# Kernel tuning notes

Measured on AMD Instinct MI355X. Metric: run time of the kernel, lower is better.

## Reference

```python
import jax, jax.numpy as jnp
import numpy as np

GAMMA = 5.0 / 3.0
N, H = 131072, 256


def mlp(c, W1, b1, W2, b2, W3, b3, W4, b4):
    h = jnp.tanh(c @ W1 + b1)
    h = jnp.tanh(h @ W2 + b2)
    h = jnp.tanh(h @ W3 + b3)
    return h @ W4 + b4  # [N, 6] -> (rho, vx, vy, Bx, By, P)


def setup_inputs() -> dict:
    key = jax.random.key(0)
    ks = jax.random.split(key, 6)
    s = 0.5
    return {
        "coords": jax.random.uniform(ks[0], (N, 3), jnp.float32),  # (x, y, t)
        "W1": jax.random.normal(ks[1], (3, H), jnp.float32) * s,
        "b1": jnp.zeros((H,), jnp.float32),
        "W2": jax.random.normal(ks[2], (H, H), jnp.float32) * (s / np.sqrt(H)),
        "b2": jnp.zeros((H,), jnp.float32),
        "W3": jax.random.normal(ks[3], (H, H), jnp.float32) * (s / np.sqrt(H)),
        "b3": jnp.zeros((H,), jnp.float32),
        "W4": jax.random.normal(ks[4], (H, 6), jnp.float32) * (s / np.sqrt(H)),
        "b4": jnp.zeros((6,), jnp.float32),
        "weights": jnp.ones((7,), jnp.float32),
    }


def reference(coords, W1, b1, W2, b2, W3, b3, W4, b4, weights):
    f = lambda c: mlp(c, W1, b1, W2, b2, W3, b3, W4, b4)
    preds = f(coords)
    # Batched Jacobian d preds / d coords via 3 forward-mode JVPs (basis dirs x,y,t)
    eye = jnp.eye(3, dtype=coords.dtype)
    jvp1 = lambda e: jax.jvp(f, (coords,), (jnp.broadcast_to(e, coords.shape),))[1]
    J = jnp.transpose(jax.vmap(jvp1)(eye), (1, 2, 0))  # [N, 6, 3]

    rho, vx, vy, Bx, By, P = (preds[:, k] for k in range(6))
    Jx, Jy, Jt = J[..., 0], J[..., 1], J[..., 2]  # each [N, 6]

    # time derivatives (chain rule for composite fields)
    dt_rho = Jt[:, 0]
    dt_Bx, dt_By = Jt[:, 3], Jt[:, 4]
    dt_rhovx = dt_rho * vx + rho * Jt[:, 1]
    dt_rhovy = dt_rho * vy + rho * Jt[:, 2]

    def dE(Jc):  # derivative of total energy E along coord c
        return (Jc[:, 5] / (GAMMA - 1.0)
                + 0.5 * Jc[:, 0] * (vx ** 2 + vy ** 2)
                + rho * (vx * Jc[:, 1] + vy * Jc[:, 2])
                + Bx * Jc[:, 3] + By * Jc[:, 4])

    dE_dx, dE_dy, dE_dt = dE(Jx), dE(Jy), dE(Jt)

    div_v = Jx[:, 1] + Jy[:, 2]
    div_B = Jx[:, 3] + Jy[:, 4]
    continuity = dt_rho + rho * div_v

    # grad of total pressure P + 0.5*(Bx^2 + By^2)
    dPm_dx = Jx[:, 5] + Bx * Jx[:, 3] + By * Jx[:, 4]
    dPm_dy = Jy[:, 5] + Bx * Jy[:, 3] + By * Jy[:, 4]
    momentum_x = dt_rhovx + dPm_dx - (Bx * Jx[:, 3] + By * Jy[:, 3])
    momentum_y = dt_rhovy + dPm_dy - (Bx * Jx[:, 4] + By * Jy[:, 4])

    # induction: G = vx*By - vy*Bx
    def dG(Jc):
        return Jc[:, 1] * By + vx * Jc[:, 4] - Jc[:, 2] * Bx - vy * Jc[:, 3]

    induction_x = dt_Bx + dG(Jy)
    induction_y = dt_By - dG(Jx)

    # energy: d/dt E + div( S*v - D*B ), S = E + P + Pm, D = B.v
    E = P / (GAMMA - 1.0) + 0.5 * rho * (vx ** 2 + vy ** 2) + 0.5 * (Bx ** 2 + By ** 2)
    S = E + P + 0.5 * (Bx ** 2 + By ** 2)
    dS_dx = dE_dx + Jx[:, 5] + Bx * Jx[:, 3] + By * Jx[:, 4]
    dS_dy = dE_dy + Jy[:, 5] + Bx * Jy[:, 3] + By * Jy[:, 4]
    D = Bx * vx + By * vy

    def dD(Jc):
        return Jc[:, 3] * vx + Bx * Jc[:, 1] + Jc[:, 4] * vy + By * Jc[:, 2]

    dFx_dx = dS_dx * vx + S * Jx[:, 1] - dD(Jx) * Bx - D * Jx[:, 3]
    dFy_dy = dS_dy * vy + S * Jy[:, 2] - dD(Jy) * By - D * Jy[:, 4]
    energy = dE_dt + dFx_dx + dFy_dy

    res = [continuity, momentum_x, momentum_y, induction_x, induction_y, energy, div_B]
    loss = sum(w * jnp.mean(r ** 2) for w, r in zip(weights, res))
    return loss
```

## Files before the change

kernel.cpp:

```cpp
#include <hip/hip_runtime.h>
#include <hip/hip_bf16.h>
#include <cstdint>


#define LDW 264
#define TPTS 16
#define GRIDB 256

typedef __attribute__((ext_vector_type(8))) short v8h;
typedef __attribute__((ext_vector_type(4))) float v4f;

__device__ __forceinline__ ushort f2b(float f) {
    uint32_t u = __float_as_uint(f);
    u = (u + 0x7fffu + ((u >> 16) & 1u)) >> 16;
    return (ushort)u;
}
__device__ __forceinline__ uint32_t pk2(float a, float b) {
    union { __hip_bfloat162 h2; uint32_t u; } cv;
    cv.h2 = __float22bfloat162_rn(make_float2(a, b));
    return cv.u;
}
__device__ __forceinline__ float fast_tanh(float x) {
    float e = __expf(2.0f * x);
    return 1.0f - 2.0f * __builtin_amdgcn_rcpf(e + 1.0f);
}

__global__ void prep_weights(const float* __restrict__ W2, const float* __restrict__ W3,
                             const float* __restrict__ W4,
                             ushort* __restrict__ Wt2, ushort* __restrict__ Wt3,
                             ushort* __restrict__ Wt4) {
    int idx = blockIdx.x * 256 + threadIdx.x;
    if (idx < 65536) {
        int k = idx >> 8, n = idx & 255;
        Wt2[n * 256 + k] = f2b(W2[k * 256 + n]);
        Wt3[n * 256 + k] = f2b(W3[k * 256 + n]);
    }
    if (idx < 4096) {
        int n = idx >> 8, k = idx & 255;
        Wt4[n * 256 + k] = (n < 6) ? f2b(W4[k * 6 + n]) : (ushort)0;
    }
}

__device__ __forceinline__ void dense_layer(const ushort* __restrict__ src,
                                            ushort* __restrict__ dst,
                                            const v8h (*wf)[8], const v4f* bs,
                                            int wv, int q, int l15) {
    v4f acc[2][4];
    #pragma unroll
    for (int a = 0; a < 2; a++)
        #pragma unroll
        for (int b = 0; b < 4; b++) {
            v4f z = {0.0f, 0.0f, 0.0f, 0.0f};
            acc[a][b] = z;
        }
    #pragma unroll
    for (int kk = 0; kk < 8; kk++) {
        v8h B[4];
        #pragma unroll
        for (int nt = 0; nt < 4; nt++)
            B[nt] = *(const v8h*)(&src[(nt * 16 + l15) * LDW + kk * 32 + q * 8]);
        #pragma unroll
        for (int mt = 0; mt < 2; mt++)
            #pragma unroll
            for (int nt = 0; nt < 4; nt++)
                acc[mt][nt] = __builtin_amdgcn_mfma_f32_16x16x32_bf16(wf[mt][kk], B[nt], acc[mt][nt], 0, 0, 0);
    }
    #pragma unroll
    for (int mt = 0; mt < 2; mt++) {
        const int colb = wv * 32 + mt * 16 + q * 4;
        v4f bb = bs[mt];
        float h0 = fast_tanh(acc[mt][0][0] + bb[0]);
        float h1 = fast_tanh(acc[mt][0][1] + bb[1]);
        float h2 = fast_tanh(acc[mt][0][2] + bb[2]);
        float h3 = fast_tanh(acc[mt][0][3] + bb[3]);
        float d0 = 1.0f - h0 * h0, d1 = 1.0f - h1 * h1;
        float d2 = 1.0f - h2 * h2, d3 = 1.0f - h3 * h3;
        uint2 w;
        w.x = pk2(h0, h1); w.y = pk2(h2, h3);
        *(uint2*)(&dst[l15 * LDW + colb]) = w;
        #pragma unroll
        for (int s = 1; s < 4; s++) {
            w.x = pk2(d0 * acc[mt][s][0], d1 * acc[mt][s][1]);
            w.y = pk2(d2 * acc[mt][s][2], d3 * acc[mt][s][3]);
            *(uint2*)(&dst[(s * 16 + l15) * LDW + colb]) = w;
        }
    }
}

__global__ __launch_bounds__(512, 2)
void mhd_fused(const float* __restrict__ coords,
               const float* __restrict__ W1, const float* __restrict__ b1,
               const float* __restrict__ b2, const float* __restrict__ b3,
               const float* __restrict__ b4,
               const float* __restrict__ wts,
               const ushort* __restrict__ Wt2, const ushort* __restrict__ Wt3,
               const ushort* __restrict__ Wt4,
               float* __restrict__ out, int npts, float inv_n) {
    __shared__ ushort Xs0[64 * LDW];
    __shared__ ushort Xs1[64 * LDW];
    __shared__ ushort W4s[16 * LDW];
    __shared__ float  cs[TPTS * 3];
    __shared__ float  Y4[4][TPTS][8];

    const int tid  = threadIdx.x;
    const int lane = tid & 63;
    const int wv   = tid >> 6;
    const int q    = lane >> 4;
    const int l15  = lane & 15;

    for (int idx = tid; idx < 16 * 256; idx += 512)
        W4s[(idx >> 8) * LDW + (idx & 255)] = Wt4[idx];

    v8h w2f[2][8], w3f[2][8];
    v4f bs2[2], bs3[2];
    #pragma unroll
    for (int mt = 0; mt < 2; mt++) {
        const int nrow = (wv * 32 + mt * 16 + l15) * 256 + q * 8;
        #pragma unroll
        for (int kk = 0; kk < 8; kk++) {
            w2f[mt][kk] = *(const v8h*)(&Wt2[nrow + kk * 32]);
            w3f[mt][kk] = *(const v8h*)(&Wt3[nrow + kk * 32]);
        }
        bs2[mt] = *(const v4f*)(&b2[wv * 32 + mt * 16 + q * 4]);
        bs3[mt] = *(const v4f*)(&b3[wv * 32 + mt * 16 + q * 4]);
    }

    const int jj = tid & 255, ph = tid >> 8;
    const float l1w0 = W1[jj], l1w1 = W1[256 + jj], l1w2 = W1[512 + jj], l1b = b1[jj];
    const float b40 = b4[0], b41 = b4[1], b42 = b4[2], b43 = b4[3], b44 = b4[4], b45 = b4[5];
    const float wt0 = wts[0], wt1 = wts[1], wt2_ = wts[2], wt3_ = wts[3],
                wt4_ = wts[4], wt5 = wts[5], wt6 = wts[6];

    const int ntiles = (npts + TPTS - 1) / TPTS;
    float vsum = 0.0f;

    for (int tile = blockIdx.x; tile < ntiles; tile += GRIDB) {
        const int base = tile * TPTS;

        if (tid < TPTS * 3) {
            int p = tid / 3, c = tid % 3;
            int gp = base + p; if (gp >= npts) gp = npts - 1;
            cs[tid] = coords[gp * 3 + c];
        }
        __syncthreads();

        #pragma unroll
        for (int pp = 0; pp < 8; pp++) {
            const int p = ph * 8 + pp;
            float x = cs[p * 3], y = cs[p * 3 + 1], t = cs[p * 3 + 2];
            float pre = fmaf(x, l1w0, fmaf(y, l1w1, fmaf(t, l1w2, l1b)));
            float h = fast_tanh(pre);
            float d = 1.0f - h * h;
            Xs0[p * LDW + jj]        = f2b(h);
            Xs0[(16 + p) * LDW + jj] = f2b(d * l1w0);
            Xs0[(32 + p) * LDW + jj] = f2b(d * l1w1);
            Xs0[(48 + p) * LDW + jj] = f2b(d * l1w2);
        }
        __syncthreads();

        dense_layer(Xs0, Xs1, w2f, bs2, wv, q, l15);
        __syncthreads();
        dense_layer(Xs1, Xs0, w3f, bs3, wv, q, l15);
        __syncthreads();

        if (wv < 4) {
            v4f a4 = {0.0f, 0.0f, 0.0f, 0.0f};
            #pragma unroll
            for (int kk = 0; kk < 8; kk++) {
                v8h A = *(const v8h*)(&W4s[l15 * LDW + kk * 32 + q * 8]);
                v8h B = *(const v8h*)(&Xs0[(wv * 16 + l15) * LDW + kk * 32 + q * 8]);
                a4 = __builtin_amdgcn_mfma_f32_16x16x32_bf16(A, B, a4, 0, 0, 0);
            }
            if (q < 2) {
                #pragma unroll
                for (int r = 0; r < 4; r++)
                    Y4[wv][l15][q * 4 + r] = a4[r];
            }
        }
        __syncthreads();

        if (tid < 16 && (base + tid) < npts) {
            const float* Yh = Y4[0][tid];
            const float* JX = Y4[1][tid];
            const float* JY = Y4[2][tid];
            const float* JT = Y4[3][tid];
            const float g1 = 1.5f;
            float rho = Yh[0] + b40, vx = Yh[1] + b41, vy = Yh[2] + b42;
            float Bx  = Yh[3] + b43, By = Yh[4] + b44, P  = Yh[5] + b45;
            float v2 = vx * vx + vy * vy;
            float dt_rho = JT[0];
            float dt_rhovx = dt_rho * vx + rho * JT[1];
            float dt_rhovy = dt_rho * vy + rho * JT[2];
            auto dE = [&](const float* J) {
                return J[5] * g1 + 0.5f * J[0] * v2 + rho * (vx * J[1] + vy * J[2]) + Bx * J[3] + By * J[4];
            };
            float dE_dx = dE(JX), dE_dy = dE(JY), dE_dt = dE(JT);
            float div_v = JX[1] + JY[2];
            float div_B = JX[3] + JY[4];
            float continuity = dt_rho + rho * div_v;
            float dPm_dx = JX[5] + Bx * JX[3] + By * JX[4];
            float dPm_dy = JY[5] + Bx * JY[3] + By * JY[4];
            float momentum_x = dt_rhovx + dPm_dx - (Bx * JX[3] + By * JY[3]);
            float momentum_y = dt_rhovy + dPm_dy - (Bx * JX[4] + By * JY[4]);
            auto dG = [&](const float* J) {
                return J[1] * By + vx * J[4] - J[2] * Bx - vy * J[3];
            };
            float induction_x = JT[3] + dG(JY);
            float induction_y = JT[4] - dG(JX);
            float E = P * g1 + 0.5f * rho * v2 + 0.5f * (Bx * Bx + By * By);
            float S = E + P + 0.5f * (Bx * Bx + By * By);
            float dS_dx = dE_dx + JX[5] + Bx * JX[3] + By * JX[4];
            float dS_dy = dE_dy + JY[5] + Bx * JY[3] + By * JY[4];
            float D = Bx * vx + By * vy;
            auto dD = [&](const float* J) {
                return J[3] * vx + Bx * J[1] + J[4] * vy + By * J[2];
            };
            float dFx_dx = dS_dx * vx + S * JX[1] - dD(JX) * Bx - D * JX[3];
            float dFy_dy = dS_dy * vy + S * JY[2] - dD(JY) * By - D * JY[4];
            float energy = dE_dt + dFx_dx + dFy_dy;
            vsum += wt0 * continuity * continuity
                  + wt1 * momentum_x * momentum_x
                  + wt2_ * momentum_y * momentum_y
                  + wt3_ * induction_x * induction_x
                  + wt4_ * induction_y * induction_y
                  + wt5 * energy * energy
                  + wt6 * div_B * div_B;
        }
    }

    if (tid < 64) {
        #pragma unroll
        for (int off = 8; off >= 1; off >>= 1)
            vsum += __shfl_down(vsum, off, 64);
        if (tid == 0) atomicAdd(out, vsum * inv_n);
    }
}

extern "C" void kernel_launch(void* const* d_in, const int* in_sizes, int n_in,
                              void* d_out, int out_size, void* d_ws, size_t ws_size,
                              hipStream_t stream) {
    const float* coords = (const float*)d_in[0];
    const float* W1 = (const float*)d_in[1];
    const float* b1 = (const float*)d_in[2];
    const float* W2 = (const float*)d_in[3];
    const float* b2 = (const float*)d_in[4];
    const float* W3 = (const float*)d_in[5];
    const float* b3 = (const float*)d_in[6];
    const float* W4 = (const float*)d_in[7];
    const float* b4 = (const float*)d_in[8];
    const float* wts = (const float*)d_in[9];
    const int npts = in_sizes[0] / 3;

    ushort* Wt2 = (ushort*)d_ws;
    ushort* Wt3 = Wt2 + 65536;
    ushort* Wt4 = Wt3 + 65536;

    hipMemsetAsync(d_out, 0, sizeof(float), stream);
    prep_weights<<<256, 256, 0, stream>>>(W2, W3, W4, Wt2, Wt3, Wt4);
    mhd_fused<<<GRIDB, 512, 0, stream>>>(coords, W1, b1, b2, b3, b4, wts,
                                         Wt2, Wt3, Wt4, (float*)d_out, npts, 1.0f / npts);
}
```

Before: 247.9 us.

## Pipeline layers 2 and 3 across warp groups with double-buffered activations

Splits the 8 waves into two groups: waves 0-3 compute layer 2 for tile i while waves 4-7 compute layer 3 for tile i-1, each group holding only its own layer's weights in registers (64 output columns per wave). Layer-2 output is double-buffered in LDS, and the next tile's coordinates are prefetched during the layer-4 stage. This cuts the number of barriers per tile and removes the serial layer2→layer3 dependency. In exchange it uses more LDS (4 activation buffers instead of 2), which may reduce occupancy, and adds a pipeline prologue and epilogue iteration.

New measurement: 259.5 us. 1.05x slower.

```diff
diff --git a/kernel.cpp b/kernel.cpp
--- a/kernel.cpp
+++ b/kernel.cpp
@@ -41,52 +41,6 @@
     }
 }
 
-__device__ __forceinline__ void dense_layer(const ushort* __restrict__ src,
-                                            ushort* __restrict__ dst,
-                                            const v8h (*wf)[8], const v4f* bs,
-                                            int wv, int q, int l15) {
-    v4f acc[2][4];
-    #pragma unroll
-    for (int a = 0; a < 2; a++)
-        #pragma unroll
-        for (int b = 0; b < 4; b++) {
-            v4f z = {0.0f, 0.0f, 0.0f, 0.0f};
-            acc[a][b] = z;
-        }
-    #pragma unroll
-    for (int kk = 0; kk < 8; kk++) {
-        v8h B[4];
-        #pragma unroll
-        for (int nt = 0; nt < 4; nt++)
-            B[nt] = *(const v8h*)(&src[(nt * 16 + l15) * LDW + kk * 32 + q * 8]);
-        #pragma unroll
-        for (int mt = 0; mt < 2; mt++)
-            #pragma unroll
-            for (int nt = 0; nt < 4; nt++)
-                acc[mt][nt] = __builtin_amdgcn_mfma_f32_16x16x32_bf16(wf[mt][kk], B[nt], acc[mt][nt], 0, 0, 0);
-    }
-    #pragma unroll
-    for (int mt = 0; mt < 2; mt++) {
-        const int colb = wv * 32 + mt * 16 + q * 4;
-        v4f bb = bs[mt];
-        float h0 = fast_tanh(acc[mt][0][0] + bb[0]);
-        float h1 = fast_tanh(acc[mt][0][1] + bb[1]);
-        float h2 = fast_tanh(acc[mt][0][2] + bb[2]);
-        float h3 = fast_tanh(acc[mt][0][3] + bb[3]);
-        float d0 = 1.0f - h0 * h0, d1 = 1.0f - h1 * h1;
-        float d2 = 1.0f - h2 * h2, d3 = 1.0f - h3 * h3;
-        uint2 w;
-        w.x = pk2(h0, h1); w.y = pk2(h2, h3);
-        *(uint2*)(&dst[l15 * LDW + colb]) = w;
-        #pragma unroll
-        for (int s = 1; s < 4; s++) {
-            w.x = pk2(d0 * acc[mt][s][0], d1 * acc[mt][s][1]);
-            w.y = pk2(d2 * acc[mt][s][2], d3 * acc[mt][s][3]);
-            *(uint2*)(&dst[(s * 16 + l15) * LDW + colb]) = w;
-        }
-    }
-}
-
 __global__ __launch_bounds__(512, 2)
 void mhd_fused(const float* __restrict__ coords,
                const float* __restrict__ W1, const float* __restrict__ b1,
@@ -96,8 +50,9 @@
                const ushort* __restrict__ Wt2, const ushort* __restrict__ Wt3,
                const ushort* __restrict__ Wt4,
                float* __restrict__ out, int npts, float inv_n) {
-    __shared__ ushort Xs0[64 * LDW];
-    __shared__ ushort Xs1[64 * LDW];
+    __shared__ ushort XsA[64 * LDW];
+    __shared__ ushort XsB[2][64 * LDW];
+    __shared__ ushort XsC[64 * LDW];
     __shared__ ushort W4s[16 * LDW];
     __shared__ float  cs[TPTS * 3];
     __shared__ float  Y4[4][TPTS][8];
@@ -107,124 +62,182 @@
     const int wv   = tid >> 6;
     const int q    = lane >> 4;
     const int l15  = lane & 15;
+    const int g3   = wv >> 2;
+    const int wvg  = wv & 3;
 
     for (int idx = tid; idx < 16 * 256; idx += 512)
         W4s[(idx >> 8) * LDW + (idx & 255)] = Wt4[idx];
 
-    v8h w2f[2][8], w3f[2][8];
-    v4f bs2[2], bs3[2];
+    const ushort* Wsrc = g3 ? Wt3 : Wt2;
+    const float*  bsrc = g3 ? b3  : b2;
+    v8h wf[4][8];
     #pragma unroll
-    for (int mt = 0; mt < 2; mt++) {
-        const int nrow = (wv * 32 + mt * 16 + l15) * 256 + q * 8;
+    for (int mt = 0; mt < 4; mt++) {
+        const int nrow = (wvg * 64 + mt * 16 + l15) * 256 + q * 8;
         #pragma unroll
-        for (int kk = 0; kk < 8; kk++) {
-            w2f[mt][kk] = *(const v8h*)(&Wt2[nrow + kk * 32]);
-            w3f[mt][kk] = *(const v8h*)(&Wt3[nrow + kk * 32]);
-        }
-        bs2[mt] = *(const v4f*)(&b2[wv * 32 + mt * 16 + q * 4]);
-        bs3[mt] = *(const v4f*)(&b3[wv * 32 + mt * 16 + q * 4]);
+        for (int kk = 0; kk < 8; kk++)
+            wf[mt][kk] = *(const v8h*)(&Wsrc[nrow + kk * 32]);
     }
 
     const int jj = tid & 255, ph = tid >> 8;
     const float l1w0 = W1[jj], l1w1 = W1[256 + jj], l1w2 = W1[512 + jj], l1b = b1[jj];
-    const float b40 = b4[0], b41 = b4[1], b42 = b4[2], b43 = b4[3], b44 = b4[4], b45 = b4[5];
-    const float wt0 = wts[0], wt1 = wts[1], wt2_ = wts[2], wt3_ = wts[3],
-                wt4_ = wts[4], wt5 = wts[5], wt6 = wts[6];
 
     const int ntiles = (npts + TPTS - 1) / TPTS;
+    const int nt_blk = (ntiles > (int)blockIdx.x)
+                         ? (ntiles - (int)blockIdx.x + GRIDB - 1) / GRIDB : 0;
+
     float vsum = 0.0f;
 
-    for (int tile = blockIdx.x; tile < ntiles; tile += GRIDB) {
-        const int base = tile * TPTS;
-
-        if (tid < TPTS * 3) {
-            int p = tid / 3, c = tid % 3;
-            int gp = base + p; if (gp >= npts) gp = npts - 1;
-            cs[tid] = coords[gp * 3 + c];
+    if (tid < TPTS * 3 && nt_blk > 0) {
+        int p = tid / 3, c = tid % 3;
+        int gp = (int)blockIdx.x * TPTS + p; if (gp >= npts) gp = npts - 1;
+        cs[tid] = coords[gp * 3 + c];
+    }
+    __syncthreads();
+
+    for (int i = 0; i <= nt_blk; ++i) {
+        const int base = ((int)blockIdx.x + i * GRIDB) * TPTS;
+
+        if (i < nt_blk) {
+            #pragma unroll
+            for (int pp = 0; pp < 8; pp++) {
+                const int p = ph * 8 + pp;
+                float x = cs[p * 3], y = cs[p * 3 + 1], t = cs[p * 3 + 2];
+                float pre = fmaf(x, l1w0, fmaf(y, l1w1, fmaf(t, l1w2, l1b)));
+                float h = fast_tanh(pre);
+                float d = 1.0f - h * h;
+                XsA[p * LDW + jj]        = f2b(h);
+                XsA[(16 + p) * LDW + jj] = f2b(d * l1w0);
+                XsA[(32 + p) * LDW + jj] = f2b(d * l1w1);
+                XsA[(48 + p) * LDW + jj] = f2b(d * l1w2);
+            }
         }
         __syncthreads();
 
-        #pragma unroll
-        for (int pp = 0; pp < 8; pp++) {
-            const int p = ph * 8 + pp;
-            float x = cs[p * 3], y = cs[p * 3 + 1], t = cs[p * 3 + 2];
-            float pre = fmaf(x, l1w0, fmaf(y, l1w1, fmaf(t, l1w2, l1b)));
-            float h = fast_tanh(pre);
-            float d = 1.0f - h * h;
-            Xs0[p * LDW + jj]        = f2b(h);
-            Xs0[(16 + p) * LDW + jj] = f2b(d * l1w0);
-            Xs0[(32 + p) * LDW + jj] = f2b(d * l1w1);
-            Xs0[(48 + p) * LDW + jj] = f2b(d * l1w2);
+        {
+            const ushort* src = g3 ? XsB[(i + 1) & 1] : XsA;
+            ushort*       dst = g3 ? XsC : XsB[i & 1];
+            const bool act = g3 ? (i >= 1) : (i < nt_blk);
+            if (act) {
+                v4f acc[4][4];
+                #pragma unroll
+                for (int a = 0; a < 4; a++)
+                    #pragma unroll
+                    for (int b = 0; b < 4; b++) {
+                        v4f z = {0.0f, 0.0f, 0.0f, 0.0f};
+                        acc[a][b] = z;
+                    }
+                #pragma unroll
+                for (int kk = 0; kk < 8; kk++) {
+                    v8h B[4];
+                    #pragma unroll
+                    for (int nt = 0; nt < 4; nt++)
+                        B[nt] = *(const v8h*)(&src[(nt * 16 + l15) * LDW + kk * 32 + q * 8]);
+                    #pragma unroll
+                    for (int mt = 0; mt < 4; mt++)
+                        #pragma unroll
+                        for (int nt = 0; nt < 4; nt++)
+                            acc[mt][nt] = __builtin_amdgcn_mfma_f32_16x16x32_bf16(
+                                              wf[mt][kk], B[nt], acc[mt][nt], 0, 0, 0);
+                }
+                #pragma unroll
+                for (int mt = 0; mt < 4; mt++) {
+                    const int nb = wvg * 64 + mt * 16 + q * 4;
+                    v4f bb = *(const v4f*)(&bsrc[nb]);
+                    float h0 = fast_tanh(acc[mt][0][0] + bb[0]);
+                    float h1 = fast_tanh(acc[mt][0][1] + bb[1]);
+                    float h2 = fast_tanh(acc[mt][0][2] + bb[2]);
+                    float h3 = fast_tanh(acc[mt][0][3] + bb[3]);
+                    float d0 = 1.0f - h0 * h0, d1 = 1.0f - h1 * h1;
+                    float d2 = 1.0f - h2 * h2, d3 = 1.0f - h3 * h3;
+                    uint2 w;
+                    w.x = pk2(h0, h1); w.y = pk2(h2, h3);
+                    *(uint2*)(&dst[l15 * LDW + nb]) = w;
+                    #pragma unroll
+                    for (int s = 1; s < 4; s++) {
+                        w.x = pk2(d0 * acc[mt][s][0], d1 * acc[mt][s][1]);
+                        w.y = pk2(d2 * acc[mt][s][2], d3 * acc[mt][s][3]);
+                        *(uint2*)(&dst[(s * 16 + l15) * LDW + nb]) = w;
+                    }
+                }
+            }
         }
         __syncthreads();
 
-        dense_layer(Xs0, Xs1, w2f, bs2, wv, q, l15);
-        __syncthreads();
-        dense_layer(Xs1, Xs0, w3f, bs3, wv, q, l15);
-        __syncthreads();
-
-        if (wv < 4) {
+        if (g3 && i >= 1) {
             v4f a4 = {0.0f, 0.0f, 0.0f, 0.0f};
             #pragma unroll
             for (int kk = 0; kk < 8; kk++) {
-                v8h A = *(const v8h*)(&W4s[l15 * LDW + kk * 32 + q * 8]);
-                v8h B = *(const v8h*)(&Xs0[(wv * 16 + l15) * LDW + kk * 32 + q * 8]);
-                a4 = __builtin_amdgcn_mfma_f32_16x16x32_bf16(A, B, a4, 0, 0, 0);
+                v8h A  = *(const v8h*)(&W4s[l15 * LDW + kk * 32 + q * 8]);
+                v8h Bf = *(const v8h*)(&XsC[(wvg * 16 + l15) * LDW + kk * 32 + q * 8]);
+                a4 = __builtin_amdgcn_mfma_f32_16x16x32_bf16(A, Bf, a4, 0, 0, 0);
             }
             if (q < 2) {
                 #pragma unroll
                 for (int r = 0; r < 4; r++)
-                    Y4[wv][l15][q * 4 + r] = a4[r];
-            }
+                    Y4[wvg][l15][q * 4 + r] = a4[r];
+            }
+        }
+        if (tid < TPTS * 3 && (i + 1) < nt_blk) {
+            int p = tid / 3, c = tid % 3;
+            int gp = base + GRIDB * TPTS + p; if (gp >= npts) gp = npts - 1;
+            cs[tid] = coords[gp * 3 + c];
         }
         __syncthreads();
 
-        if (tid < 16 && (base + tid) < npts) {
-            const float* Yh = Y4[0][tid];
-            const float* JX = Y4[1][tid];
-            const float* JY = Y4[2][tid];
-            const float* JT = Y4[3][tid];
-            const float g1 = 1.5f;
-            float rho = Yh[0] + b40, vx = Yh[1] + b41, vy = Yh[2] + b42;
-            float Bx  = Yh[3] + b43, By = Yh[4] + b44, P  = Yh[5] + b45;
-            float v2 = vx * vx + vy * vy;
-            float dt_rho = JT[0];
-            float dt_rhovx = dt_rho * vx + rho * JT[1];
-            float dt_rhovy = dt_rho * vy + rho * JT[2];
-            auto dE = [&](const float* J) {
-                return J[5] * g1 + 0.5f * J[0] * v2 + rho * (vx * J[1] + vy * J[2]) + Bx * J[3] + By * J[4];
-            };
-            float dE_dx = dE(JX), dE_dy = dE(JY), dE_dt = dE(JT);
-            float div_v = JX[1] + JY[2];
-            float div_B = JX[3] + JY[4];
-            float continuity = dt_rho + rho * div_v;
-            float dPm_dx = JX[5] + Bx * JX[3] + By * JX[4];
-            float dPm_dy = JY[5] + Bx * JY[3] + By * JY[4];
-            float momentum_x = dt_rhovx + dPm_dx - (Bx * JX[3] + By * JY[3]);
-            float momentum_y = dt_rhovy + dPm_dy - (Bx * JX[4] + By * JY[4]);
-            auto dG = [&](const float* J) {
-                return J[1] * By + vx * J[4] - J[2] * Bx - vy * J[3];
-            };
-            float induction_x = JT[3] + dG(JY);
-            float induction_y = JT[4] - dG(JX);
-            float E = P * g1 + 0.5f * rho * v2 + 0.5f * (Bx * Bx + By * By);
-            float S = E + P + 0.5f * (Bx * Bx + By * By);
-            float dS_dx = dE_dx + JX[5] + Bx * JX[3] + By * JX[4];
-            float dS_dy = dE_dy + JY[5] + Bx * JY[3] + By * JY[4];
-            float D = Bx * vx + By * vy;
-            auto dD = [&](const float* J) {
-                return J[3] * vx + Bx * J[1] + J[4] * vy + By * J[2];
-            };
-            float dFx_dx = dS_dx * vx + S * JX[1] - dD(JX) * Bx - D * JX[3];
-            float dFy_dy = dS_dy * vy + S * JY[2] - dD(JY) * By - D * JY[4];
-            float energy = dE_dt + dFx_dx + dFy_dy;
-            vsum += wt0 * continuity * continuity
-                  + wt1 * momentum_x * momentum_x
-                  + wt2_ * momentum_y * momentum_y
-                  + wt3_ * induction_x * induction_x
-                  + wt4_ * induction_y * induction_y
-                  + wt5 * energy * energy
-                  + wt6 * div_B * div_B;
+        if (i >= 1 && tid < 16) {
+            const int pb = base - GRIDB * TPTS;
+            if (pb + tid < npts) {
+                const float* Yh = Y4[0][tid];
+                const float* JX = Y4[1][tid];
+                const float* JY = Y4[2][tid];
+                const float* JT = Y4[3][tid];
+                const float b40 = b4[0], b41 = b4[1], b42 = b4[2],
+                            b43 = b4[3], b44 = b4[4], b45 = b4[5];
+                const float wt0 = wts[0], wt1 = wts[1], wt2_ = wts[2], wt3_ = wts[3],
+                            wt4_ = wts[4], wt5 = wts[5], wt6 = wts[6];
+                const float g1 = 1.5f;
+                float rho = Yh[0] + b40, vx = Yh[1] + b41, vy = Yh[2] + b42;
+                float Bx  = Yh[3] + b43, By = Yh[4] + b44, P  = Yh[5] + b45;
+                float v2 = vx * vx + vy * vy;
+                float dt_rho = JT[0];
+                float dt_rhovx = dt_rho * vx + rho * JT[1];
+                float dt_rhovy = dt_rho * vy + rho * JT[2];
+                auto dE = [&](const float* J) {
+                    return J[5] * g1 + 0.5f * J[0] * v2 + rho * (vx * J[1] + vy * J[2]) + Bx * J[3] + By * J[4];
+                };
+                float dE_dx = dE(JX), dE_dy = dE(JY), dE_dt = dE(JT);
+                float div_v = JX[1] + JY[2];
+                float div_B = JX[3] + JY[4];
+                float continuity = dt_rho + rho * div_v;
+                float dPm_dx = JX[5] + Bx * JX[3] + By * JX[4];
+                float dPm_dy = JY[5] + Bx * JY[3] + By * JY[4];
+                float momentum_x = dt_rhovx + dPm_dx - (Bx * JX[3] + By * JY[3]);
+                float momentum_y = dt_rhovy + dPm_dy - (Bx * JX[4] + By * JY[4]);
+                auto dG = [&](const float* J) {
+                    return J[1] * By + vx * J[4] - J[2] * Bx - vy * J[3];
+                };
+                float induction_x = JT[3] + dG(JY);
+                float induction_y = JT[4] - dG(JX);
+                float E = P * g1 + 0.5f * rho * v2 + 0.5f * (Bx * Bx + By * By);
+                float S = E + P + 0.5f * (Bx * Bx + By * By);
+                float dS_dx = dE_dx + JX[5] + Bx * JX[3] + By * JX[4];
+                float dS_dy = dE_dy + JY[5] + Bx * JY[3] + By * JY[4];
+                float D = Bx * vx + By * vy;
+                auto dD = [&](const float* J) {
+                    return J[3] * vx + Bx * J[1] + J[4] * vy + By * J[2];
+                };
+                float dFx_dx = dS_dx * vx + S * JX[1] - dD(JX) * Bx - D * JX[3];
+                float dFy_dy = dS_dy * vy + S * JY[2] - dD(JY) * By - D * JY[4];
+                float energy = dE_dt + dFx_dx + dFy_dy;
+                vsum += wt0 * continuity * continuity
+                      + wt1 * momentum_x * momentum_x
+                      + wt2_ * momentum_y * momentum_y
+                      + wt3_ * induction_x * induction_x
+                      + wt4_ * induction_y * induction_y
+                      + wt5 * energy * energy
+                      + wt6 * div_B * div_B;
+            }
         }
     }
 
```
